# Optimization experiments

Measured on AMD Instinct MI355X. Metric: run time of the kernel, lower is better.

The kernel has to match this reference:

```python
import jax, jax.numpy as jnp
import numpy as np

B, T, D, E, C = 2, 2048, 2048, 8, 512
O1 = D // E  # per-expert hidden width (out_features // num_experts)


def setup_inputs() -> dict:
    key = jax.random.key(0)
    k = jax.random.split(key, 8)
    s = 1.0 / np.sqrt(D)
    return {
        "x": jax.random.normal(k[0], (B, T, D), dtype=jnp.float32),
        "dispatch_mask": jax.random.uniform(k[1], (B, T, E, C), dtype=jnp.float32),
        "combine_array": jax.random.uniform(k[2], (B, T, E, C), dtype=jnp.float32),
        # contract weights: nn.Linear(D, D) reshaped to (E, D//E, D)
        "W1": jax.random.uniform(k[3], (E, O1, D), jnp.float32, -s, s),
        "b1": jax.random.uniform(k[4], (E, O1), jnp.float32, -s, s),
        # expand weights: nn.Linear(D, D) reshaped to (E, D, D//E)
        "W2": jax.random.uniform(k[5], (E, D, O1), jnp.float32, -s, s),
        "b2": jax.random.uniform(k[6], (D,), jnp.float32, -s, s),
    }


def reference(x, dispatch_mask, combine_array, W1, b1, W2, b2):
    # --- ExpertsChooseMaskedContract ---
    # einsum('btd,btec,eod->beco') split into two GEMM-shaped contractions
    xe = jnp.einsum('btd,btec->becd', x, dispatch_mask)          # [B,E,C,D]
    h = jnp.einsum('becd,eod->beco', xe, W1) + b1[None, :, None, :]  # [B,E,C,O1]
    # --- GELU (torch nn.GELU default = exact erf form) ---
    h = jax.nn.gelu(h, approximate=False)
    # --- ExpertsChooseMaskedExpand (homogeneous-coords bias == add b2 then combine) ---
    y = jnp.einsum('beci,eoi->beco', h, W2) + b2[None, None, None, :]  # [B,E,C,D]
    out = jnp.einsum('beco,btec->bto', y, combine_array)          # [B,T,D]
    return out
```

## Files before the change

kernel.cpp:

```cpp
#include <hip/hip_runtime.h>
#include <math.h>

#define BB 2
#define TT 2048
#define DD 2048
#define EE 8
#define CCv 512
#define OO1 256

typedef unsigned short u16;
typedef __bf16 bf16x8 __attribute__((ext_vector_type(8)));
typedef float f32x4 __attribute__((ext_vector_type(4)));

__device__ __forceinline__ u16 f2bf(float f) {
    unsigned u = __float_as_uint(f);
    unsigned r = (u + 0x7fffu + ((u >> 16) & 1u)) >> 16;
    return (u16)r;
}

__device__ __forceinline__ void gload16(const void* g, void* s) {
    __builtin_amdgcn_global_load_lds(
        (const __attribute__((address_space(1))) void*)g,
        (__attribute__((address_space(3))) void*)s, 16, 0, 0);
}

__global__ __launch_bounds__(256) void conv_cast(const float* __restrict__ in,
                                                 u16* __restrict__ out, long n) {
    long i = ((long)blockIdx.x * 256 + threadIdx.x) * 4;
    float4 v = *(const float4*)&in[i];
    ushort4 o; o.x = f2bf(v.x); o.y = f2bf(v.y); o.z = f2bf(v.z); o.w = f2bf(v.w);
    *(ushort4*)&out[i] = o;
}

__global__ __launch_bounds__(256) void add_inplace(float* __restrict__ out,
                                                   const float* __restrict__ part) {
    long i = ((long)blockIdx.x * 256 + threadIdx.x) * 4;
    float4 a = *(float4*)&out[i];
    float4 b = *(const float4*)&part[i];
    a.x += b.x; a.y += b.y; a.z += b.z; a.w += b.w;
    *(float4*)&out[i] = a;
}

__global__ __launch_bounds__(256) void transpose_conv(
    const float* __restrict__ in, long inHi, long inLo, int modZ, long sIn,
    u16* __restrict__ out, long outZ, long sOut)
{
    __shared__ float tile[32][33];
    const int z = blockIdx.z;
    const float* ib = in + (long)(z / modZ) * inHi + (long)(z % modZ) * inLo;
    u16* ob = out + (long)z * outZ;
    const int t0 = blockIdx.y * 32, c0 = blockIdx.x * 32;
    const int tid = threadIdx.x;
    const int r = tid >> 3, c4 = (tid & 7) * 4;

    float4 v = *(const float4*)&ib[(long)(t0 + r) * sIn + c0 + c4];
    tile[r][c4 + 0] = v.x; tile[r][c4 + 1] = v.y;
    tile[r][c4 + 2] = v.z; tile[r][c4 + 3] = v.w;
    __syncthreads();

    const int oc = tid >> 3, t4 = (tid & 7) * 4;
    ushort4 o;
    o.x = f2bf(tile[t4 + 0][oc]);
    o.y = f2bf(tile[t4 + 1][oc]);
    o.z = f2bf(tile[t4 + 2][oc]);
    o.w = f2bf(tile[t4 + 3][oc]);
    *(ushort4*)&ob[(long)(c0 + oc) * sOut + t0 + t4] = o;
}

template<int EPI>
__global__ __launch_bounds__(256)
void mfma_gemm(const u16* __restrict__ A, long ldA, long aHi, long aLo, int modA,
               const u16* __restrict__ B, long ldB, long bHi, long bLo, int modB,
               void* __restrict__ Cout, long ldC, long cHi, long cLo, int modC,
               const float* __restrict__ bias, long biasLo, int modBias,
               int M, int N, int K)
{
    __shared__ __align__(16) char smem[32768];
    char* smA = smem;
    char* smB = smem + 16384;

    const int z = blockIdx.z;
    const char* Ab = (const char*)(A + (long)(z / modA) * aHi + (long)(z % modA) * aLo);
    const char* Bb = (const char*)(B + (long)(z / modB) * bHi + (long)(z % modB) * bLo);
    const long ldAb = ldA * 2, ldBb = ldB * 2;

    const int m0 = blockIdx.y * 128, n0 = blockIdx.x * 128;
    const int tid = threadIdx.x;
    const int l = tid & 63;
    const int w = tid >> 6;
    const int wm = w >> 1, wn = w & 1;

    const int srow = l >> 3;
    const int schunk = (l & 7) ^ srow;
    const int frow = l & 15;
    const int fgrp = l >> 4;
    const int fch0 = fgrp ^ (l & 7);

    int aoff[4], boff[4];
#pragma unroll
    for (int i = 0; i < 4; ++i) {
        aoff[i] = (wm * 64 + i * 16 + frow) * 128 + fch0 * 16;
        boff[i] = (wn * 64 + i * 16 + frow) * 128 + fch0 * 16;
    }

    f32x4 acc[4][4];
    const f32x4 zero4 = {0.f, 0.f, 0.f, 0.f};
#pragma unroll
    for (int i = 0; i < 4; ++i)
#pragma unroll
        for (int j = 0; j < 4; ++j) acc[i][j] = zero4;

    const long sgo = (long)schunk * 16;

    for (int k0 = 0; k0 < K; k0 += 64) {
        const long kb = (long)k0 * 2;
#pragma unroll
        for (int j = 0; j < 4; ++j) {
            const int rr = (j * 4 + w) * 8 + srow;
            gload16(Ab + (long)(m0 + rr) * ldAb + kb + sgo, smA + (j * 4 + w) * 1024);
            gload16(Bb + (long)(n0 + rr) * ldBb + kb + sgo, smB + (j * 4 + w) * 1024);
        }
        __syncthreads();
#pragma unroll
        for (int kk = 0; kk < 2; ++kk) {
            const int kx = kk * 64;
            bf16x8 af[4], bfr[4];
#pragma unroll
            for (int i = 0; i < 4; ++i) af[i] = *(const bf16x8*)(smA + (aoff[i] ^ kx));
#pragma unroll
            for (int i = 0; i < 4; ++i) bfr[i] = *(const bf16x8*)(smB + (boff[i] ^ kx));
#pragma unroll
            for (int mi = 0; mi < 4; ++mi)
#pragma unroll
                for (int ni = 0; ni < 4; ++ni)
                    acc[mi][ni] = __builtin_amdgcn_mfma_f32_16x16x32_bf16(
                        af[mi], bfr[ni], acc[mi][ni], 0, 0, 0);
        }
        __syncthreads();
    }

    const long cbase = (long)(z / modC) * cHi + (long)(z % modC) * cLo;
    const float* biasB = bias + (long)(z % modBias) * biasLo;
#pragma unroll
    for (int mi = 0; mi < 4; ++mi) {
#pragma unroll
        for (int ni = 0; ni < 4; ++ni) {
            const int col = n0 + wn * 64 + ni * 16 + frow;
            const int rowb = m0 + wm * 64 + mi * 16 + fgrp * 4;
#pragma unroll
            for (int r = 0; r < 4; ++r) {
                float v = acc[mi][ni][r];
                const int row = rowb + r;
                if (EPI == 1) {
                    v += biasB[col];
                    v = 0.5f * v * (1.0f + erff(v * 0.70710678118654752f));
                } else {
                    v += biasB[row];
                }
                ((u16*)Cout)[cbase + (long)row * ldC + col] = f2bf(v);
            }
        }
    }
}

template<int OUTBF>
__global__ __launch_bounds__(512, 2)
void mfma_gemm_256(const u16* __restrict__ A, long ldA, long aHi, long aLo, int modA,
                   const u16* __restrict__ B, long ldB, long bHi, long bLo, int modB,
                   void* __restrict__ Cout, long ldC, long cHi, long cLo, int modC,
                   int M, int N, int K)
{
    __shared__ __align__(16) char smem[131072];

    const int z = blockIdx.z;
    const char* Ab = (const char*)(A + (long)(z / modA) * aHi + (long)(z % modA) * aLo);
    const char* Bb = (const char*)(B + (long)(z / modB) * bHi + (long)(z % modB) * bLo);
    const long ldAb = ldA * 2, ldBb = ldB * 2;

    const int m0 = blockIdx.y * 256, n0 = blockIdx.x * 256;
    const int tid = threadIdx.x;
    const int l = tid & 63;
    const int w = tid >> 6;
    const int wm = w >> 2, wn = w & 3;

    const int srow = l >> 3;
    const int schunk = (l & 7) ^ srow;
    const long sgo = (long)schunk * 16;
    const int frow = l & 15, fgrp = l >> 4;
    const int cs0 = (fgrp ^ (l & 7)) * 16;

    auto stage = [&](int kt, int bsel, int half, int j) {
        const int rr = (w * 2 + j) * 8 + srow;
        const char* gb = (half < 2) ? Ab : Bb;
        const long ld = (half < 2) ? ldAb : ldBb;
        const int gr = ((half < 2) ? m0 + half * 128 : n0 + (half - 2) * 128) + rr;
        gload16(gb + (long)gr * ld + (long)kt * 128 + sgo,
                smem + bsel * 65536 + half * 16384 + (w * 2 + j) * 1024);
    };

    f32x4 acc[2][4][2][2];
    const f32x4 zero4 = {0.f, 0.f, 0.f, 0.f};
#pragma unroll
    for (int qm = 0; qm < 2; ++qm)
#pragma unroll
        for (int mi = 0; mi < 4; ++mi)
#pragma unroll
            for (int qn = 0; qn < 2; ++qn)
#pragma unroll
                for (int ni = 0; ni < 2; ++ni) acc[qm][mi][qn][ni] = zero4;

    int aoff[4], boff[2];
#pragma unroll
    for (int mi = 0; mi < 4; ++mi) aoff[mi] = (wm * 64 + mi * 16 + frow) * 128 + cs0;
#pragma unroll
    for (int ni = 0; ni < 2; ++ni) boff[ni] = (wn * 32 + ni * 16 + frow) * 128 + cs0;

    stage(0, 0, 0, 0); stage(0, 0, 0, 1);
    stage(0, 0, 2, 0); stage(0, 0, 2, 1);
    stage(0, 0, 3, 0); stage(0, 0, 3, 1);
    stage(0, 0, 1, 0); stage(0, 0, 1, 1);

    const int NT = K >> 6;
    for (int kt = 0; kt < NT; ++kt) {
        const char* buf = smem + (kt & 1) * 65536;
        const int sb = (kt & 1) ^ 1;
        const bool pf = (kt + 1) < NT;

        asm volatile("s_waitcnt vmcnt(0)" ::: "memory");
        __builtin_amdgcn_s_barrier();

        if (pf) {
            const int kn = kt + 1;
            stage(kn, sb, 0, 0); stage(kn, sb, 0, 1);
            stage(kn, sb, 2, 0); stage(kn, sb, 2, 1);
            stage(kn, sb, 3, 0); stage(kn, sb, 3, 1);
            stage(kn, sb, 1, 0); stage(kn, sb, 1, 1);
        }

        bf16x8 af[4][2], bq0[2][2], bq1[2][2];

#pragma unroll
        for (int mi = 0; mi < 4; ++mi) {
            af[mi][0] = *(const bf16x8*)(buf + aoff[mi]);
            af[mi][1] = *(const bf16x8*)(buf + (aoff[mi] ^ 64));
        }
#pragma unroll
        for (int ni = 0; ni < 2; ++ni) {
            bq0[ni][0] = *(const bf16x8*)(buf + 32768 + boff[ni]);
            bq0[ni][1] = *(const bf16x8*)(buf + 32768 + (boff[ni] ^ 64));
        }
        asm volatile("s_waitcnt lgkmcnt(0)" ::: "memory");
        __builtin_amdgcn_sched_barrier(0);
        __builtin_amdgcn_s_setprio(1);
#pragma unroll
        for (int kk = 0; kk < 2; ++kk)
#pragma unroll
            for (int mi = 0; mi < 4; ++mi)
#pragma unroll
                for (int ni = 0; ni < 2; ++ni)
                    acc[0][mi][0][ni] = __builtin_amdgcn_mfma_f32_16x16x32_bf16(
                        af[mi][kk], bq0[ni][kk], acc[0][mi][0][ni], 0, 0, 0);
        __builtin_amdgcn_s_setprio(0);

#pragma unroll
        for (int ni = 0; ni < 2; ++ni) {
            bq1[ni][0] = *(const bf16x8*)(buf + 49152 + boff[ni]);
            bq1[ni][1] = *(const bf16x8*)(buf + 49152 + (boff[ni] ^ 64));
        }
        asm volatile("s_waitcnt lgkmcnt(0)" ::: "memory");
        __builtin_amdgcn_sched_barrier(0);
        __builtin_amdgcn_s_setprio(1);
#pragma unroll
        for (int kk = 0; kk < 2; ++kk)
#pragma unroll
            for (int mi = 0; mi < 4; ++mi)
#pragma unroll
                for (int ni = 0; ni < 2; ++ni)
                    acc[0][mi][1][ni] = __builtin_amdgcn_mfma_f32_16x16x32_bf16(
                        af[mi][kk], bq1[ni][kk], acc[0][mi][1][ni], 0, 0, 0);
        __builtin_amdgcn_s_setprio(0);

#pragma unroll
        for (int mi = 0; mi < 4; ++mi) {
            af[mi][0] = *(const bf16x8*)(buf + 16384 + aoff[mi]);
            af[mi][1] = *(const bf16x8*)(buf + 16384 + (aoff[mi] ^ 64));
        }
        asm volatile("s_waitcnt lgkmcnt(0)" ::: "memory");
        __builtin_amdgcn_sched_barrier(0);
        __builtin_amdgcn_s_setprio(1);
#pragma unroll
        for (int kk = 0; kk < 2; ++kk)
#pragma unroll
            for (int mi = 0; mi < 4; ++mi)
#pragma unroll
                for (int ni = 0; ni < 2; ++ni)
                    acc[1][mi][1][ni] = __builtin_amdgcn_mfma_f32_16x16x32_bf16(
                        af[mi][kk], bq1[ni][kk], acc[1][mi][1][ni], 0, 0, 0);
        __builtin_amdgcn_s_setprio(0);

        __builtin_amdgcn_s_setprio(1);
#pragma unroll
        for (int kk = 0; kk < 2; ++kk)
#pragma unroll
            for (int mi = 0; mi < 4; ++mi)
#pragma unroll
                for (int ni = 0; ni < 2; ++ni)
                    acc[1][mi][0][ni] = __builtin_amdgcn_mfma_f32_16x16x32_bf16(
                        af[mi][kk], bq0[ni][kk], acc[1][mi][0][ni], 0, 0, 0);
        __builtin_amdgcn_s_setprio(0);
    }

    const long cbase = (long)(z / modC) * cHi + (long)(z % modC) * cLo;
#pragma unroll
    for (int qm = 0; qm < 2; ++qm)
#pragma unroll
        for (int mi = 0; mi < 4; ++mi)
#pragma unroll
            for (int qn = 0; qn < 2; ++qn)
#pragma unroll
                for (int ni = 0; ni < 2; ++ni) {
                    const int col = n0 + qn * 128 + wn * 32 + ni * 16 + frow;
                    const int rowb = m0 + qm * 128 + wm * 64 + mi * 16 + fgrp * 4;
#pragma unroll
                    for (int r = 0; r < 4; ++r) {
                        const float v = acc[qm][mi][qn][ni][r];
                        const long idx = cbase + (long)(rowb + r) * ldC + col;
                        if (OUTBF) ((u16*)Cout)[idx] = f2bf(v);
                        else       ((float*)Cout)[idx] = v;
                    }
                }
}

extern "C" void kernel_launch(void* const* d_in, const int* in_sizes, int n_in,
                              void* d_out, int out_size, void* d_ws, size_t ws_size,
                              hipStream_t stream) {
    const float* x    = (const float*)d_in[0];
    const float* mask = (const float*)d_in[1];
    const float* comb = (const float*)d_in[2];
    const float* W1   = (const float*)d_in[3];
    const float* b1   = (const float*)d_in[4];
    const float* W2   = (const float*)d_in[5];
    const float* b2   = (const float*)d_in[6];
    float* out = (float*)d_out;

    char* ws = (char*)d_ws;
    u16* buf0 = (u16*)ws;
    u16* xT   = (u16*)(ws + 33554432);
    u16* W1b  = (u16*)(ws + 50331648);
    u16* W2b  = (u16*)(ws + 58720256);
    u16* xe   = (u16*)(ws + 67108864);
    u16* h    = (u16*)(ws + 100663296);
    u16* yT   = xe;
    float* part = (float*)(ws + 33554432);

    transpose_conv<<<dim3(DD / 32, TT / 32, BB), 256, 0, stream>>>(
        x, (long)TT * DD, 0L, 1, (long)DD, xT, (long)DD * TT, (long)TT);
    transpose_conv<<<dim3(CCv / 32, TT / 32, BB * EE), 256, 0, stream>>>(
        mask, (long)TT * EE * CCv, (long)CCv, EE, (long)EE * CCv,
        buf0, (long)CCv * TT, (long)TT);
    conv_cast<<<(int)((8L * OO1 * DD) / 1024), 256, 0, stream>>>(W1, W1b, 8L * OO1 * DD);
    conv_cast<<<(int)((8L * DD * OO1) / 1024), 256, 0, stream>>>(W2, W2b, 8L * DD * OO1);

    mfma_gemm_256<1><<<dim3(DD / 256, CCv / 256, 16), 512, 0, stream>>>(
        buf0, 2048, 1048576L, 0L, 1,
        xT,   2048, 4194304L, 0L, 8,
        xe,   2048, 1048576L, 0L, 1,
        CCv, DD, TT);

    conv_cast<<<(int)((2L * TT * EE * CCv) / 1024), 256, 0, stream>>>(
        comb, buf0, 2L * TT * EE * CCv);

    mfma_gemm<1><<<dim3(OO1 / 128, CCv / 128, 16), 256, 0, stream>>>(
        xe,  2048, 1048576L, 0L, 1,
        W1b, 2048, 0L, 524288L, 8,
        h,   256, 131072L, 0L, 1,
        b1, 256L, 8, CCv, OO1, DD);

    mfma_gemm<3><<<dim3(CCv / 128, DD / 128, 16), 256, 0, stream>>>(
        W2b, 256, 0L, 524288L, 8,
        h,   256, 131072L, 0L, 1,
        yT,  4096, 8388608L, 512L, 8,
        b2, 0L, 1, DD, CCv, OO1);

    const long dPart = (long)((char*)part - (char*)out) / 4;
    mfma_gemm_256<0><<<dim3(DD / 256, TT / 256, 4), 512, 0, stream>>>(
        buf0, 4096, 2048L, 8388608L, 2,
        yT,   4096, 2048L, 8388608L, 2,
        out,  2048, dPart, 4194304L, 2,
        TT, DD, 2048);
    add_inplace<<<8192, 256, 0, stream>>>(out, part);
}
```

Before: 276.7 us.

## Restructure 256-tile GEMM mainloop into 8-phase pipelined schedule with interleaved prefetch

Replaces the per-k-tile loop, which waited for all global loads at its top and then issued the next tile's loads in one burst, with a two-tile unrolled loop. The loop interleaves LDS fragment reads, quarter-tile global-to-LDS stages for the next tiles and MFMA clusters, separated by barriers. Partial vmcnt waits keep up to six loads in flight across iterations, aiming to hide global latency behind compute. It adds many more workgroup barriers per tile, and it assumes an even number of k-tiles.

```diff
diff --git a/kernel.cpp b/kernel.cpp
--- a/kernel.cpp
+++ b/kernel.cpp
@@ -163,6 +163,10 @@
     }
 }
 
+#define PH_FENCE() \
+    asm volatile("s_waitcnt lgkmcnt(0)" ::: "memory"); \
+    __builtin_amdgcn_sched_barrier(0)
+
 template<int OUTBF>
 __global__ __launch_bounds__(512, 2)
 void mfma_gemm_256(const u16* __restrict__ A, long ldA, long aHi, long aLo, int modA,
@@ -219,96 +223,127 @@
     stage(0, 0, 2, 0); stage(0, 0, 2, 1);
     stage(0, 0, 3, 0); stage(0, 0, 3, 1);
     stage(0, 0, 1, 0); stage(0, 0, 1, 1);
+    stage(1, 1, 0, 0); stage(1, 1, 0, 1);
+    stage(1, 1, 2, 0); stage(1, 1, 2, 1);
+    stage(1, 1, 3, 0); stage(1, 1, 3, 1);
+    asm volatile("s_waitcnt vmcnt(6)" ::: "memory");
+    __builtin_amdgcn_s_barrier();
 
     const int NT = K >> 6;
-    for (int kt = 0; kt < NT; ++kt) {
-        const char* buf = smem + (kt & 1) * 65536;
-        const int sb = (kt & 1) ^ 1;
-        const bool pf = (kt + 1) < NT;
-
-        asm volatile("s_waitcnt vmcnt(0)" ::: "memory");
-        __builtin_amdgcn_s_barrier();
-
-        if (pf) {
-            const int kn = kt + 1;
-            stage(kn, sb, 0, 0); stage(kn, sb, 0, 1);
-            stage(kn, sb, 2, 0); stage(kn, sb, 2, 1);
-            stage(kn, sb, 3, 0); stage(kn, sb, 3, 1);
-            stage(kn, sb, 1, 0); stage(kn, sb, 1, 1);
-        }
-
+    const int NI = NT >> 1;
+    const char* b0 = smem;
+    const char* b1 = smem + 65536;
+
+#define MFMA16(QM, QN, AFR, BQ) \
+    __builtin_amdgcn_s_setprio(1); \
+    _Pragma("unroll") \
+    for (int kk = 0; kk < 2; ++kk) \
+        _Pragma("unroll") \
+        for (int mi = 0; mi < 4; ++mi) \
+            _Pragma("unroll") \
+            for (int ni = 0; ni < 2; ++ni) \
+                acc[QM][mi][QN][ni] = __builtin_amdgcn_mfma_f32_16x16x32_bf16( \
+                    AFR[mi][kk], BQ[ni][kk], acc[QM][mi][QN][ni], 0, 0, 0); \
+    __builtin_amdgcn_s_setprio(0)
+
+    for (int it = 0; it < NI; ++it) {
+        const int t1 = 2 * it + 1, t2 = t1 + 1, t3 = t1 + 2;
+        const bool pf = t2 < NT;
         bf16x8 af[4][2], bq0[2][2], bq1[2][2];
 
 #pragma unroll
         for (int mi = 0; mi < 4; ++mi) {
-            af[mi][0] = *(const bf16x8*)(buf + aoff[mi]);
-            af[mi][1] = *(const bf16x8*)(buf + (aoff[mi] ^ 64));
+            af[mi][0] = *(const bf16x8*)(b0 + aoff[mi]);
+            af[mi][1] = *(const bf16x8*)(b0 + (aoff[mi] ^ 64));
         }
 #pragma unroll
         for (int ni = 0; ni < 2; ++ni) {
-            bq0[ni][0] = *(const bf16x8*)(buf + 32768 + boff[ni]);
-            bq0[ni][1] = *(const bf16x8*)(buf + 32768 + (boff[ni] ^ 64));
-        }
-        asm volatile("s_waitcnt lgkmcnt(0)" ::: "memory");
+            bq0[ni][0] = *(const bf16x8*)(b0 + 32768 + boff[ni]);
+            bq0[ni][1] = *(const bf16x8*)(b0 + 32768 + (boff[ni] ^ 64));
+        }
+        stage(t1, 1, 1, 0); stage(t1, 1, 1, 1);
+        __builtin_amdgcn_s_barrier();
+        PH_FENCE();
+        MFMA16(0, 0, af, bq0);
+        __builtin_amdgcn_s_barrier();
+
+#pragma unroll
+        for (int ni = 0; ni < 2; ++ni) {
+            bq1[ni][0] = *(const bf16x8*)(b0 + 49152 + boff[ni]);
+            bq1[ni][1] = *(const bf16x8*)(b0 + 49152 + (boff[ni] ^ 64));
+        }
+        if (pf) { stage(t2, 0, 0, 0); stage(t2, 0, 0, 1); }
+        __builtin_amdgcn_s_barrier();
+        PH_FENCE();
+        MFMA16(0, 1, af, bq1);
+        __builtin_amdgcn_s_barrier();
+
+#pragma unroll
+        for (int mi = 0; mi < 4; ++mi) {
+            af[mi][0] = *(const bf16x8*)(b0 + 16384 + aoff[mi]);
+            af[mi][1] = *(const bf16x8*)(b0 + 16384 + (aoff[mi] ^ 64));
+        }
+        if (pf) { stage(t2, 0, 2, 0); stage(t2, 0, 2, 1); }
+        __builtin_amdgcn_s_barrier();
+        PH_FENCE();
+        MFMA16(1, 1, af, bq1);
+        __builtin_amdgcn_s_barrier();
+
+        if (pf) { stage(t2, 0, 3, 0); stage(t2, 0, 3, 1); }
+        __builtin_amdgcn_s_barrier();
         __builtin_amdgcn_sched_barrier(0);
-        __builtin_amdgcn_s_setprio(1);
-#pragma unroll
-        for (int kk = 0; kk < 2; ++kk)
-#pragma unroll
-            for (int mi = 0; mi < 4; ++mi)
-#pragma unroll
-                for (int ni = 0; ni < 2; ++ni)
-                    acc[0][mi][0][ni] = __builtin_amdgcn_mfma_f32_16x16x32_bf16(
-                        af[mi][kk], bq0[ni][kk], acc[0][mi][0][ni], 0, 0, 0);
-        __builtin_amdgcn_s_setprio(0);
-
+        MFMA16(1, 0, af, bq0);
+        if (pf) { asm volatile("s_waitcnt vmcnt(6)" ::: "memory"); }
+        else    { asm volatile("s_waitcnt vmcnt(0)" ::: "memory"); }
+        __builtin_amdgcn_s_barrier();
+
+#pragma unroll
+        for (int mi = 0; mi < 4; ++mi) {
+            af[mi][0] = *(const bf16x8*)(b1 + aoff[mi]);
+            af[mi][1] = *(const bf16x8*)(b1 + (aoff[mi] ^ 64));
+        }
 #pragma unroll
         for (int ni = 0; ni < 2; ++ni) {
-            bq1[ni][0] = *(const bf16x8*)(buf + 49152 + boff[ni]);
-            bq1[ni][1] = *(const bf16x8*)(buf + 49152 + (boff[ni] ^ 64));
-        }
-        asm volatile("s_waitcnt lgkmcnt(0)" ::: "memory");
+            bq0[ni][0] = *(const bf16x8*)(b1 + 32768 + boff[ni]);
+            bq0[ni][1] = *(const bf16x8*)(b1 + 32768 + (boff[ni] ^ 64));
+        }
+        if (pf) { stage(t2, 0, 1, 0); stage(t2, 0, 1, 1); }
+        __builtin_amdgcn_s_barrier();
+        PH_FENCE();
+        MFMA16(0, 0, af, bq0);
+        __builtin_amdgcn_s_barrier();
+
+#pragma unroll
+        for (int ni = 0; ni < 2; ++ni) {
+            bq1[ni][0] = *(const bf16x8*)(b1 + 49152 + boff[ni]);
+            bq1[ni][1] = *(const bf16x8*)(b1 + 49152 + (boff[ni] ^ 64));
+        }
+        if (pf) { stage(t3, 1, 0, 0); stage(t3, 1, 0, 1); }
+        __builtin_amdgcn_s_barrier();
+        PH_FENCE();
+        MFMA16(0, 1, af, bq1);
+        __builtin_amdgcn_s_barrier();
+
+#pragma unroll
+        for (int mi = 0; mi < 4; ++mi) {
+            af[mi][0] = *(const bf16x8*)(b1 + 16384 + aoff[mi]);
+            af[mi][1] = *(const bf16x8*)(b1 + 16384 + (aoff[mi] ^ 64));
+        }
+        if (pf) { stage(t3, 1, 2, 0); stage(t3, 1, 2, 1); }
+        __builtin_amdgcn_s_barrier();
+        PH_FENCE();
+        MFMA16(1, 1, af, bq1);
+        __builtin_amdgcn_s_barrier();
+
+        if (pf) { stage(t3, 1, 3, 0); stage(t3, 1, 3, 1); }
+        __builtin_amdgcn_s_barrier();
         __builtin_amdgcn_sched_barrier(0);
-        __builtin_amdgcn_s_setprio(1);
-#pragma unroll
-        for (int kk = 0; kk < 2; ++kk)
-#pragma unroll
-            for (int mi = 0; mi < 4; ++mi)
-#pragma unroll
-                for (int ni = 0; ni < 2; ++ni)
-                    acc[0][mi][1][ni] = __builtin_amdgcn_mfma_f32_16x16x32_bf16(
-                        af[mi][kk], bq1[ni][kk], acc[0][mi][1][ni], 0, 0, 0);
-        __builtin_amdgcn_s_setprio(0);
-
-#pragma unroll
-        for (int mi = 0; mi < 4; ++mi) {
-            af[mi][0] = *(const bf16x8*)(buf + 16384 + aoff[mi]);
-            af[mi][1] = *(const bf16x8*)(buf + 16384 + (aoff[mi] ^ 64));
-        }
-        asm volatile("s_waitcnt lgkmcnt(0)" ::: "memory");
-        __builtin_amdgcn_sched_barrier(0);
-        __builtin_amdgcn_s_setprio(1);
-#pragma unroll
-        for (int kk = 0; kk < 2; ++kk)
-#pragma unroll
-            for (int mi = 0; mi < 4; ++mi)
-#pragma unroll
-                for (int ni = 0; ni < 2; ++ni)
-                    acc[1][mi][1][ni] = __builtin_amdgcn_mfma_f32_16x16x32_bf16(
-                        af[mi][kk], bq1[ni][kk], acc[1][mi][1][ni], 0, 0, 0);
-        __builtin_amdgcn_s_setprio(0);
-
-        __builtin_amdgcn_s_setprio(1);
-#pragma unroll
-        for (int kk = 0; kk < 2; ++kk)
-#pragma unroll
-            for (int mi = 0; mi < 4; ++mi)
-#pragma unroll
-                for (int ni = 0; ni < 2; ++ni)
-                    acc[1][mi][0][ni] = __builtin_amdgcn_mfma_f32_16x16x32_bf16(
-                        af[mi][kk], bq0[ni][kk], acc[1][mi][0][ni], 0, 0, 0);
-        __builtin_amdgcn_s_setprio(0);
+        MFMA16(1, 0, af, bq0);
+        if (pf) { asm volatile("s_waitcnt vmcnt(6)" ::: "memory"); }
+        else    { asm volatile("s_waitcnt vmcnt(0)" ::: "memory"); }
+        __builtin_amdgcn_s_barrier();
     }
+#undef MFMA16
 
     const long cbase = (long)(z / modC) * cHi + (long)(z % modC) * cLo;
 #pragma unroll
```

New measurement: 278.0 us. About the same (+0.5%).
